# Kernel tuning notes

Measured on AMD Instinct MI355X. Metric: run time of the kernel, lower is better.

## Reference

```python
import jax, jax.numpy as jnp
import numpy as np

N = 4096       # nodes
E = 131072     # edges (avg degree 32)
IN_C = 512
HID = 512
OUT_C = 64
RANK = 64      # svd_q
N_DOM = 4
EPS = 1e-5     # BatchNorm eps


def setup_inputs() -> dict:
    key = jax.random.key(0)
    ks = jax.random.split(key, 12)
    x = jax.random.normal(ks[0], (N, IN_C), dtype=jnp.float32)
    row = jax.random.randint(ks[1], (E,), 0, N)
    off = jax.random.randint(ks[2], (E,), 1, N)
    col = (row + off) % N  # guarantee no pre-existing self loops
    edge_index = jnp.stack([row, col]).astype(jnp.int32)
    edge_weight = jax.random.uniform(ks[3], (E,), dtype=jnp.float32)
    y = jax.random.randint(ks[4], (N,), 0, N_DOM).astype(jnp.int32)
    W1 = jax.random.normal(ks[5], (IN_C, HID), dtype=jnp.float32) / np.sqrt(IN_C).astype(np.float32)
    b1 = jnp.zeros((HID,), jnp.float32)
    Wmu = jax.random.normal(ks[6], (HID, OUT_C), dtype=jnp.float32) / np.sqrt(HID).astype(np.float32)
    bmu = jnp.zeros((OUT_C,), jnp.float32)
    Wlv = jax.random.normal(ks[7], (HID, OUT_C), dtype=jnp.float32) / np.sqrt(HID).astype(np.float32)
    blv = jnp.zeros((OUT_C,), jnp.float32)
    gamma = jnp.ones((N_DOM, HID), jnp.float32)   # per-domain BN weight
    beta = jnp.zeros((N_DOM, HID), jnp.float32)   # per-domain BN bias
    return dict(x=x, edge_index=edge_index, edge_weight=edge_weight, y=y,
                W1=W1, b1=b1, Wmu=Wmu, bmu=bmu, Wlv=Wlv, blv=blv,
                gamma=gamma, beta=beta)


def _safe_rsqrt(deg):
    # PyG gcn_norm: deg^-0.5 with inf (and here non-positive) masked to 0
    safe = jnp.where(deg > 0, deg, 1.0)
    return jnp.where(deg > 0, 1.0 / jnp.sqrt(safe), 0.0)


def gcn_conv_edges(x, W, b, row, col, w, n):
    # GCNConv with edge weights: add remaining self loops (fill=1), symmetric norm
    loop = jnp.arange(n, dtype=row.dtype)
    row_f = jnp.concatenate([row, loop])
    col_f = jnp.concatenate([col, loop])
    w_f = jnp.concatenate([w, jnp.ones((n,), w.dtype)])
    deg = jax.ops.segment_sum(w_f, col_f, num_segments=n)
    dinv = _safe_rsqrt(deg)
    norm = dinv[row_f] * w_f * dinv[col_f]
    xw = x @ W                                   # [n, out]
    out = jax.ops.segment_sum(norm[:, None] * xw[row_f], col_f, num_segments=n)
    return out + b


def gcn_conv_dense(x, W, b, A):
    # Dense-adjacency GCNConv (reconstructed adjacency already has a diagonal,
    # so add_remaining_self_loops is a no-op). deg over target (col) index.
    deg = A.sum(axis=0)
    dinv = _safe_rsqrt(deg)
    Ahat = dinv[:, None] * A * dinv[None, :]     # [n, n] normalized
    return Ahat.T @ (x @ W) + b                  # aggregate at targets


def svd_lowrank_recon(A, q, niter=2):
    # torch.svd_lowrank-style randomized SVD, then U @ diag(s) @ V^T
    omega = jax.random.normal(jax.random.key(42), (A.shape[1], q), A.dtype)
    Qb = jnp.linalg.qr(A @ omega)[0]
    for _ in range(niter):
        Qb = jnp.linalg.qr(A.T @ Qb)[0]
        Qb = jnp.linalg.qr(A @ Qb)[0]
    B = Qb.T @ A                                 # [q, n]
    U, s, Vt = jnp.linalg.svd(B, full_matrices=False)
    return (Qb @ (U * s)) @ Vt                   # [n, n] low-rank reconstruction


def dsbn_relu(x, y, gamma, beta):
    # Domain-specific BatchNorm (training-mode batch stats per domain) + ReLU
    out = jnp.zeros_like(x)
    for i in range(N_DOM):
        m = (y == i)
        mf = m.astype(x.dtype)[:, None]
        cnt = jnp.maximum(mf.sum(), 1.0)
        mean = (x * mf).sum(0) / cnt
        var = (((x - mean) ** 2) * mf).sum(0) / cnt   # biased var, as BatchNorm
        xn = (x - mean) / jnp.sqrt(var + EPS) * gamma[i] + beta[i]
        out = jnp.where(m[:, None], xn, out)
    return jax.nn.relu(out)


def reference(x, edge_index, edge_weight, y, W1, b1, Wmu, bmu, Wlv, blv, gamma, beta):
    row, col = edge_index[0], edge_index[1]
    # ----- branch 1: original sparse graph -----
    h1 = dsbn_relu(gcn_conv_edges(x, W1, b1, row, col, edge_weight, N), y, gamma, beta)
    z_mean1 = gcn_conv_edges(h1, Wmu, bmu, row, col, edge_weight, N)
    z_log1 = gcn_conv_edges(h1, Wlv, blv, row, col, edge_weight, N)
    # ----- branch 2: SVD low-rank reconstructed (dense) graph -----
    A = jnp.zeros((N, N), x.dtype).at[row, col].add(edge_weight)  # coalesced COO
    A2 = svd_lowrank_recon(A, RANK)
    h2 = dsbn_relu(gcn_conv_dense(x, W1, b1, A2), y, gamma, beta)
    z_mean2 = gcn_conv_dense(h2, Wmu, bmu, A2)
    z_log2 = gcn_conv_dense(h2, Wlv, blv, A2)
    return (z_mean1, z_log1, z_mean2, z_log2)
```

## Files before the change

kernel.cpp:

```cpp
#include <hip/hip_runtime.h>
#include <hip/hip_bf16.h>


#define NN    4096
#define NEDG  131072
#define INC   512
#define HIDC  512
#define OUTC  64
#define RK    64
#define NDOM  4
#define EPSBN 1e-5f

typedef unsigned short ushortT;
typedef __attribute__((ext_vector_type(8))) short bf16x8;
typedef __attribute__((ext_vector_type(4))) float f32x4;

static inline int cdiv(int a, int b){ return (a + b - 1) / b; }

__device__ __forceinline__ float bf2f(unsigned u){ return __uint_as_float(u << 16); }

__global__ __launch_bounds__(256) void k_detect(const unsigned short* __restrict__ p,
                                                int* __restrict__ flag){
  int t = threadIdx.x;
  int cnt = 0;
  for (int i = t; i < 4096; i += 256){
    unsigned short v = p[2*i];
    int e = (v >> 7) & 0xFF;
    if (e >= 100 && e <= 140) cnt++;
  }
  __shared__ int sh[256];
  sh[t] = cnt; __syncthreads();
  for (int off = 128; off > 0; off >>= 1){ if (t < off) sh[t] += sh[t+off]; __syncthreads(); }
  if (t == 0) *flag = (sh[0] >= 2048) ? 0 : 1;
}

__device__ __forceinline__ float upc1(const void* s, int f, int off){
  return f ? ((const float*)s)[off]
           : __bfloat162float(((const __hip_bfloat16*)s)[off]);
}
__device__ __forceinline__ ushortT tobf(float v){
  __hip_bfloat16 h = __float2bfloat16(v);
  return *(ushortT*)&h;
}
#define SEG_X   2097152
#define SEG_W1  262144
#define SEG_W   131072
#define SEG_WMU 32768
#define SEG_GB  2048
#define SEG_B1  512
#define SEG_BO  64
#define OFF1 (SEG_X)
#define OFF2 (OFF1+SEG_W1)
#define OFF3 (OFF2+SEG_W)
#define OFF4 (OFF3+SEG_WMU)
#define OFF5 (OFF4+SEG_WMU)
#define OFF6 (OFF5+SEG_GB)
#define OFF7 (OFF6+SEG_GB)
#define OFF8 (OFF7+SEG_B1)
#define OFF9 (OFF8+SEG_BO)
#define OFFT (OFF9+SEG_BO)

__global__ __launch_bounds__(256) void k_upcast_all(
    const void* x, const void* W1, const void* w, const void* Wmu, const void* Wlv,
    const void* gm, const void* bt, const void* b1, const void* bmu, const void* blv,
    const int* __restrict__ isf32,
    float* dx, float* dW1, float* dw, float* dWmu, float* dWlv,
    float* dgm, float* dbt, float* db1, float* dbmu, float* dblv,
    ushortT* xbf, ushortT* W1bf, ushortT* Wmubf, ushortT* Wlvbf){
  int i = blockIdx.x*256 + threadIdx.x;
  if (i >= OFFT) return;
  int f = *isf32;
  if      (i < OFF1){ float v = upc1(x, f, i); dx[i] = v; xbf[i] = tobf(v); }
  else if (i < OFF2){ float v = upc1(W1, f, i - OFF1); dW1[i - OFF1] = v; W1bf[i - OFF1] = tobf(v); }
  else if (i < OFF3) dw  [i - OFF2] = upc1(w,   f, i - OFF2);
  else if (i < OFF4){ float v = upc1(Wmu, f, i - OFF3); dWmu[i - OFF3] = v; Wmubf[i - OFF3] = tobf(v); }
  else if (i < OFF5){ float v = upc1(Wlv, f, i - OFF4); dWlv[i - OFF4] = v; Wlvbf[i - OFF4] = tobf(v); }
  else if (i < OFF6) dgm [i - OFF5] = upc1(gm,  f, i - OFF5);
  else if (i < OFF7) dbt [i - OFF6] = upc1(bt,  f, i - OFF6);
  else if (i < OFF8) db1 [i - OFF7] = upc1(b1,  f, i - OFF7);
  else if (i < OFF9) dbmu[i - OFF8] = upc1(bmu, f, i - OFF8);
  else               dblv[i - OFF9] = upc1(blv, f, i - OFF9);
}

__global__ __launch_bounds__(256) void k_prep(float* deg, int* cntR, int* cntC, int* dcnt,
                                              float* bnsum){
  int i = blockIdx.x*256 + threadIdx.x;
  if (i < NN){ deg[i] = 1.0f; cntR[i] = 0; cntC[i] = 0; }
  if (i < NDOM) dcnt[i] = 0;
  if (i < 8*HIDC) bnsum[i] = 0.f;
}

__global__ __launch_bounds__(256) void k_hist(const int* __restrict__ row, const int* __restrict__ col,
                                              const float* __restrict__ w, float* deg,
                                              int* cntR, int* cntC){
  int e = blockIdx.x*256 + threadIdx.x;
  if (e < NEDG){
    atomicAdd(&deg[col[e]], w[e]);
    atomicAdd(&cntR[row[e]], 1);
    atomicAdd(&cntC[col[e]], 1);
  }
}
__global__ __launch_bounds__(256) void k_dinv(const float* deg, float* dinv, int n){
  int i = blockIdx.x*256 + threadIdx.x;
  if (i < n){ float d = deg[i]; dinv[i] = (d > 0.f) ? 1.f/sqrtf(d) : 0.f; }
}
__global__ __launch_bounds__(256) void k_norm1(const int* __restrict__ row, const int* __restrict__ col,
                                               const float* __restrict__ w, const float* __restrict__ dinv,
                                               float* __restrict__ nrm){
  int e = blockIdx.x*256 + threadIdx.x;
  if (e < NEDG) nrm[e] = dinv[row[e]] * w[e] * dinv[col[e]];
}
__global__ __launch_bounds__(1024) void k_scan4096(const int* __restrict__ cnt,
                                                   int* __restrict__ ptr, int* __restrict__ pos){
  __shared__ int sh[1024];
  int t = threadIdx.x;
  int b = t*4;
  int a0 = cnt[b], a1 = cnt[b+1], a2 = cnt[b+2], a3 = cnt[b+3];
  sh[t] = a0 + a1 + a2 + a3;
  __syncthreads();
  for (int off = 1; off < 1024; off <<= 1){
    int v = (t >= off) ? sh[t-off] : 0;
    __syncthreads();
    sh[t] += v;
    __syncthreads();
  }
  int excl = (t == 0) ? 0 : sh[t-1];
  ptr[b]   = excl;            pos[b]   = excl;
  ptr[b+1] = excl+a0;         pos[b+1] = excl+a0;
  ptr[b+2] = excl+a0+a1;      pos[b+2] = excl+a0+a1;
  ptr[b+3] = excl+a0+a1+a2;   pos[b+3] = excl+a0+a1+a2;
  if (t == 1023) ptr[4096] = sh[1023];
}
__global__ __launch_bounds__(256) void k_scatter(const int* __restrict__ row, const int* __restrict__ col,
                                                 int* posR, int* posC, int* eidR, int* eidC){
  int e = blockIdx.x*256 + threadIdx.x;
  if (e < NEDG){
    int p = atomicAdd(&posR[row[e]], 1); eidR[p] = e;
    int q = atomicAdd(&posC[col[e]], 1); eidC[q] = e;
  }
}
__global__ __launch_bounds__(256) void k_edges(const int* __restrict__ rowA, const int* __restrict__ colA,
        const float* __restrict__ wf, const float* __restrict__ nrm,
        const int* __restrict__ eidR, const int* __restrict__ eidC,
        int* __restrict__ csrSrc, float* __restrict__ csrW,
        int* __restrict__ cscSrc, float* __restrict__ cscW, float* __restrict__ cscN){
  int p = blockIdx.x*256 + threadIdx.x;
  if (p < NEDG){
    int eR = eidR[p]; csrSrc[p] = colA[eR]; csrW[p] = wf[eR];
    int eC = eidC[p]; cscSrc[p] = rowA[eC]; cscW[p] = wf[eC]; cscN[p] = nrm[eC];
  }
}
__global__ __launch_bounds__(256) void k_dcnt(const int* __restrict__ y, int* dcnt){
  int i = blockIdx.x*256 + threadIdx.x;
  if (i < NN) atomicAdd(&dcnt[y[i]], 1);
}

__device__ __forceinline__ unsigned rotl32(unsigned x, unsigned d){ return (x << d) | (x >> (32u - d)); }
#define TF_ROUND4(R0,R1,R2,R3) \
  x0 += x1; x1 = rotl32(x1,R0); x1 ^= x0; \
  x0 += x1; x1 = rotl32(x1,R1); x1 ^= x0; \
  x0 += x1; x1 = rotl32(x1,R2); x1 ^= x0; \
  x0 += x1; x1 = rotl32(x1,R3); x1 ^= x0;

__device__ __forceinline__ void tf2x32(unsigned k0, unsigned k1, unsigned c0, unsigned c1,
                                       unsigned* o0, unsigned* o1){
  unsigned ks2 = 0x1BD11BDAu ^ k0 ^ k1;
  unsigned x0 = c0 + k0, x1 = c1 + k1;
  TF_ROUND4(13,15,26,6);   x0 += k1;  x1 += ks2 + 1u;
  TF_ROUND4(17,29,16,24);  x0 += ks2; x1 += k0 + 2u;
  TF_ROUND4(13,15,26,6);   x0 += k0;  x1 += k1 + 3u;
  TF_ROUND4(17,29,16,24);  x0 += k1;  x1 += ks2 + 4u;
  TF_ROUND4(13,15,26,6);   x0 += ks2; x1 += k0 + 5u;
  *o0 = x0; *o1 = x1;
}

__device__ double erfinv64(double x){
  double w = -log1p(-x*x);
  double p;
  if (w < 5.0){
    w -= 2.5;
    p = 2.81022636e-08;  p = p*w + 3.43273939e-07; p = p*w - 3.5233877e-06;
    p = p*w - 4.39150654e-06; p = p*w + 0.00021858087; p = p*w - 0.00125372503;
    p = p*w - 0.00417768164;  p = p*w + 0.246640727;   p = p*w + 1.50140941;
  } else {
    w = sqrt(w) - 3.0;
    p = -0.000200214257; p = p*w + 0.000100950558; p = p*w + 0.00134934322;
    p = p*w - 0.00367342844; p = p*w + 0.00573950773; p = p*w - 0.0076224613;
    p = p*w + 0.00943887047; p = p*w + 1.00167406;    p = p*w + 2.83297682;
  }
  double y = p * x;
  const double c = 1.1283791670955126;
  #pragma unroll
  for (int it = 0; it < 3; it++){
    double err = erf(y) - x;
    y -= err / (c * exp(-y*y));
  }
  return y;
}

__device__ float bits_to_normal(unsigned b){
  float f = __uint_as_float((b >> 9) | 0x3f800000u) - 1.0f;
  const float lo = -0.99999994f;
  float x = fmaxf(lo, f * 2.0f + lo);
  double r = 1.4142135623730951 * erfinv64((double)x);
  return (float)r;
}

__global__ __launch_bounds__(256) void k_omega(float* __restrict__ om, double* __restrict__ Gd){
  int i = blockIdx.x*256 + threadIdx.x;
  if (i < RK*RK) Gd[i] = 0.0;
  if (i >= 262144) return;
  unsigned o0, o1;
  tf2x32(0u, 42u, 0u, (unsigned)i, &o0, &o1);
  om[i] = bits_to_normal(o0 ^ o1);
}

__global__ __launch_bounds__(256) void k_gemm_bf16(
    const ushortT* __restrict__ A, const ushortT* __restrict__ B,
    ushortT* __restrict__ Cbf){
  __shared__ ushortT As2[64][40];
  __shared__ ushortT Bs2[64][40];
  int t = threadIdx.x;
  int bm = blockIdx.y * 64, bn = blockIdx.x * 64;
  int w = t >> 6, l = t & 63;
  int lr = l & 15, lk = l >> 4;
  f32x4 acc[4] = {};
  int ar = t >> 2, ac = (t & 3) * 8;
  int bc = t & 63, bk = (t >> 6) * 8;
  for (int k0 = 0; k0 < 512; k0 += 32){
    *(uint4*)&As2[ar][ac] = *(const uint4*)&A[(size_t)(bm + ar) * 512 + k0 + ac];
    ushortT tmp[8];
    #pragma unroll
    for (int j = 0; j < 8; j++)
      tmp[j] = B[(size_t)(k0 + bk + j) * 512 + bn + bc];
    *(uint4*)&Bs2[bc][bk] = *(uint4*)tmp;
    __syncthreads();
    bf16x8 afrag = *(bf16x8*)&As2[w * 16 + lr][lk * 8];
    #pragma unroll
    for (int nt = 0; nt < 4; nt++){
      bf16x8 bfrag = *(bf16x8*)&Bs2[nt * 16 + lr][lk * 8];
      acc[nt] = __builtin_amdgcn_mfma_f32_16x16x32_bf16(afrag, bfrag, acc[nt], 0, 0, 0);
    }
    __syncthreads();
  }
  #pragma unroll
  for (int nt = 0; nt < 4; nt++){
    #pragma unroll
    for (int i = 0; i < 4; i++){
      size_t idx = (size_t)(bm + w * 16 + lk * 4 + i) * 512 + bn + nt * 16 + lr;
      Cbf[idx] = tobf(acc[nt][i]);
    }
  }
}

__device__ __forceinline__ void d_hw2(int bx, int t,
    const ushortT* __restrict__ A, const ushortT* __restrict__ Bm,
    const ushortT* __restrict__ Bl, float* __restrict__ Ca, float* __restrict__ Cb){
  __shared__ ushortT As2[64][40];
  __shared__ ushortT Bs2[64][40];
  int nb = NN/64;
  int second = bx >= nb;
  int bm = (bx - (second ? nb : 0)) * 64;
  const ushortT* B = second ? Bl : Bm;
  float* Cc = second ? Cb : Ca;
  int w = t >> 6, l = t & 63;
  int lr = l & 15, lk = l >> 4;
  f32x4 acc[4] = {};
  int ar = t >> 2, ac = (t & 3) * 8;
  int bc = t & 63, bk = (t >> 6) * 8;
  for (int k0 = 0; k0 < 512; k0 += 32){
    *(uint4*)&As2[ar][ac] = *(const uint4*)&A[(size_t)(bm + ar) * 512 + k0 + ac];
    ushortT tmp[8];
    #pragma unroll
    for (int j = 0; j < 8; j++)
      tmp[j] = B[(size_t)(k0 + bk + j) * 64 + bc];
    *(uint4*)&Bs2[bc][bk] = *(uint4*)tmp;
    __syncthreads();
    bf16x8 afrag = *(bf16x8*)&As2[w * 16 + lr][lk * 8];
    #pragma unroll
    for (int nt = 0; nt < 4; nt++){
      bf16x8 bfrag = *(bf16x8*)&Bs2[nt * 16 + lr][lk * 8];
      acc[nt] = __builtin_amdgcn_mfma_f32_16x16x32_bf16(afrag, bfrag, acc[nt], 0, 0, 0);
    }
    __syncthreads();
  }
  #pragma unroll
  for (int nt = 0; nt < 4; nt++){
    #pragma unroll
    for (int i = 0; i < 4; i++){
      Cc[(size_t)(bm + w * 16 + lk * 4 + i) * 64 + nt * 16 + lr] = acc[nt][i];
    }
  }
}
__global__ __launch_bounds__(256) void k_gemm_hw2(
    const ushortT* __restrict__ A, const ushortT* __restrict__ Bm,
    const ushortT* __restrict__ Bl, float* __restrict__ Ca, float* __restrict__ Cb){
  d_hw2(blockIdx.x, threadIdx.x, A, Bm, Bl, Ca, Cb);
}

__global__ __launch_bounds__(256) void k_gemm_nn(int M, int Nn, int K,
      const float* __restrict__ A, int lda, const float* __restrict__ B, int ldb,
      float* __restrict__ Cc, int ldc, const float* __restrict__ rowscale,
      const float* __restrict__ kscale, const float* __restrict__ bias){
  __shared__ float As[16][65];
  __shared__ float Bs[16][65];
  int bm = blockIdx.y*64, bn = blockIdx.x*64;
  int t = threadIdx.x;
  int tr = t >> 4, tc = t & 15;
  float acc[4][4] = {};
  for (int k0 = 0; k0 < K; k0 += 16){
    #pragma unroll
    for (int q = 0; q < 4; q++){
      int idx = t*4 + q;
      int m = idx >> 4, kk = idx & 15;
      As[kk][m] = A[(size_t)(bm+m)*lda + (k0+kk)];
    }
    #pragma unroll
    for (int q = 0; q < 4; q++){
      int idx = t + q*256;
      int kk = idx >> 6, n = idx & 63;
      float ks = kscale ? kscale[k0+kk] : 1.0f;
      Bs[kk][n] = B[(size_t)(k0+kk)*ldb + (bn+n)] * ks;
    }
    __syncthreads();
    #pragma unroll
    for (int kk = 0; kk < 16; kk++){
      float a0 = As[kk][tr*4+0], a1 = As[kk][tr*4+1], a2 = As[kk][tr*4+2], a3 = As[kk][tr*4+3];
      float b0 = Bs[kk][tc*4+0], b1 = Bs[kk][tc*4+1], b2 = Bs[kk][tc*4+2], b3 = Bs[kk][tc*4+3];
      acc[0][0] += a0*b0; acc[0][1] += a0*b1; acc[0][2] += a0*b2; acc[0][3] += a0*b3;
      acc[1][0] += a1*b0; acc[1][1] += a1*b1; acc[1][2] += a1*b2; acc[1][3] += a1*b3;
      acc[2][0] += a2*b0; acc[2][1] += a2*b1; acc[2][2] += a2*b2; acc[2][3] += a2*b3;
      acc[3][0] += a3*b0; acc[3][1] += a3*b1; acc[3][2] += a3*b2; acc[3][3] += a3*b3;
    }
    __syncthreads();
  }
  #pragma unroll
  for (int i2 = 0; i2 < 4; i2++){
    int m = bm + tr*4 + i2;
    float rs = rowscale ? rowscale[m] : 1.0f;
    #pragma unroll
    for (int j2 = 0; j2 < 4; j2++){
      int n = bn + tc*4 + j2;
      float v = acc[i2][j2] * rs;
      if (bias) v += bias[n];
      Cc[(size_t)m*ldc + n] = v;
    }
  }
}

__global__ __launch_bounds__(256) void k_gemm_nn2(
      const float* __restrict__ A, const float* __restrict__ Um,
      const float* __restrict__ rowscale,
      const float* __restrict__ bmu, const float* __restrict__ blv,
      float* __restrict__ zout){
  __shared__ float As[16][65];
  __shared__ float Bs[16][65];
  int z = blockIdx.z;
  const float* B = Um + (size_t)z*RK*RK;
  const float* bias = z ? blv : bmu;
  float* Cc = zout + (size_t)(2+z)*NN*OUTC;
  int bm = blockIdx.y*64;
  int t = threadIdx.x;
  int tr = t >> 4, tc = t & 15;
  float acc[4][4] = {};
  for (int k0 = 0; k0 < RK; k0 += 16){
    #pragma unroll
    for (int q = 0; q < 4; q++){
      int idx = t*4 + q;
      int m = idx >> 4, kk = idx & 15;
      As[kk][m] = A[(size_t)(bm+m)*RK + (k0+kk)];
    }
    #pragma unroll
    for (int q = 0; q < 4; q++){
      int idx = t + q*256;
      int kk = idx >> 6, n = idx & 63;
      Bs[kk][n] = B[(size_t)(k0+kk)*RK + n];
    }
    __syncthreads();
    #pragma unroll
    for (int kk = 0; kk < 16; kk++){
      float a0 = As[kk][tr*4+0], a1 = As[kk][tr*4+1], a2 = As[kk][tr*4+2], a3 = As[kk][tr*4+3];
      float b0 = Bs[kk][tc*4+0], b1 = Bs[kk][tc*4+1], b2 = Bs[kk][tc*4+2], b3 = Bs[kk][tc*4+3];
      acc[0][0] += a0*b0; acc[0][1] += a0*b1; acc[0][2] += a0*b2; acc[0][3] += a0*b3;
      acc[1][0] += a1*b0; acc[1][1] += a1*b1; acc[1][2] += a1*b2; acc[1][3] += a1*b3;
      acc[2][0] += a2*b0; acc[2][1] += a2*b1; acc[2][2] += a2*b2; acc[2][3] += a2*b3;
      acc[3][0] += a3*b0; acc[3][1] += a3*b1; acc[3][2] += a3*b2; acc[3][3] += a3*b3;
    }
    __syncthreads();
  }
  #pragma unroll
  for (int i2 = 0; i2 < 4; i2++){
    int m = bm + tr*4 + i2;
    float rs = rowscale[m];
    #pragma unroll
    for (int j2 = 0; j2 < 4; j2++){
      int n = tc*4 + j2;
      Cc[(size_t)m*OUTC + n] = acc[i2][j2] * rs + bias[n];
    }
  }
}

__global__ __launch_bounds__(256) void k_gemm_tn_bfm(
    const float* __restrict__ Bf1, const float* __restrict__ dinv2,
    const ushortT* __restrict__ xw1bf, float* __restrict__ Tm){
  __shared__ ushortT As2[64][40];
  __shared__ ushortT Bs2[64][40];
  int t = threadIdx.x;
  int bn = blockIdx.x * 64;
  int kb = blockIdx.y * 512;
  int w = t >> 6, l = t & 63;
  int lr = l & 15, lk = l >> 4;
  f32x4 acc[4] = {};
  int sc = t & 63, sk = (t >> 6) * 8;
  for (int k0 = kb; k0 < kb + 512; k0 += 32){
    ushortT tmpA[8], tmpB[8];
    #pragma unroll
    for (int j = 0; j < 8; j++){
      int krow = k0 + sk + j;
      tmpA[j] = tobf(dinv2[krow] * Bf1[(size_t)krow*RK + sc]);
      tmpB[j] = xw1bf[(size_t)krow*HIDC + bn + sc];
    }
    *(uint4*)&As2[sc][sk] = *(uint4*)tmpA;
    *(uint4*)&Bs2[sc][sk] = *(uint4*)tmpB;
    __syncthreads();
    bf16x8 afrag = *(bf16x8*)&As2[w*16 + lr][lk*8];
    #pragma unroll
    for (int nt = 0; nt < 4; nt++){
      bf16x8 bfrag = *(bf16x8*)&Bs2[nt*16 + lr][lk*8];
      acc[nt] = __builtin_amdgcn_mfma_f32_16x16x32_bf16(afrag, bfrag, acc[nt], 0, 0, 0);
    }
    __syncthreads();
  }
  #pragma unroll
  for (int nt = 0; nt < 4; nt++){
    #pragma unroll
    for (int i = 0; i < 4; i++){
      atomicAdd(&Tm[(size_t)(w*16 + lk*4 + i)*HIDC + bn + nt*16 + lr], acc[nt][i]);
    }
  }
}

__global__ __launch_bounds__(256) void k_gemm_tn_sk2(
      const float* __restrict__ A,
      const float* __restrict__ Ba, const float* __restrict__ Bb,
      float* __restrict__ Um, const float* __restrict__ kscale){
  __shared__ float As[32][17];
  __shared__ float Bs[32][17];
  int z = blockIdx.z;
  int second = z >= 16;
  int kb = (second ? z - 16 : z) * 256, ke = kb + 256;
  const float* B = second ? Bb : Ba;
  float* Cc = Um + (second ? RK*RK : 0);
  int bm = blockIdx.y*16, bn = blockIdx.x*16;
  int t = threadIdx.x;
  int tm = t >> 4, tn = t & 15;
  float acc = 0.f;
  for (int k0 = kb; k0 < ke; k0 += 32){
    #pragma unroll
    for (int q = 0; q < 2; q++){
      int idx = t + q*256;
      int kk = idx >> 4, m = idx & 15;
      As[kk][m] = A[(size_t)(k0+kk)*RK + (bm+m)] * kscale[k0+kk];
      Bs[kk][m] = B[(size_t)(k0+kk)*OUTC + (bn+m)];
    }
    __syncthreads();
    #pragma unroll
    for (int kk = 0; kk < 32; kk++) acc += As[kk][tm] * Bs[kk][tn];
    __syncthreads();
  }
  atomicAdd(&Cc[(size_t)(bm+tm)*RK + (bn+tn)], acc);
}

__global__ __launch_bounds__(64) void k_spmm32(const int* __restrict__ ptr,
                       const int* __restrict__ src, const float* __restrict__ cf,
                       const float* __restrict__ X, float* __restrict__ Y){
  int seg = blockIdx.x;
  int t = threadIdx.x;
  double acc = 0.0;
  int p0 = ptr[seg], p1 = ptr[seg+1];
  for (int p = p0; p < p1; ++p){
    acc += (double)cf[p] * (double)X[(size_t)src[p]*RK + t];
  }
  Y[(size_t)seg*RK + t] = (float)acc;
}
__global__ __launch_bounds__(64) void k_spmm32to64(const int* __restrict__ ptr,
                       const int* __restrict__ src, const float* __restrict__ cf,
                       const float* __restrict__ X, double* __restrict__ Y){
  int seg = blockIdx.x;
  int t = threadIdx.x;
  double acc = 0.0;
  int p0 = ptr[seg], p1 = ptr[seg+1];
  for (int p = p0; p < p1; ++p){
    acc += (double)cf[p] * (double)X[(size_t)src[p]*RK + t];
  }
  Y[(size_t)seg*RK + t] = acc;
}
__global__ __launch_bounds__(256) void k_gram64(const double* __restrict__ X, double* __restrict__ G){
  __shared__ double Xs[64][65];
  int b = blockIdx.x;
  int t = threadIdx.x;
  #pragma unroll
  for (int q = 0; q < 16; q++){
    int idx = t + q*256;
    Xs[idx >> 6][idx & 63] = X[(size_t)(b*64 + (idx >> 6))*RK + (idx & 63)];
  }
  __syncthreads();
  int i = t >> 2;
  int j0 = (t & 3) * 16;
  double acc[16];
  #pragma unroll
  for (int jj = 0; jj < 16; jj++) acc[jj] = 0.0;
  for (int k = 0; k < 64; k++){
    double a = Xs[k][i];
    #pragma unroll
    for (int jj = 0; jj < 16; jj++) acc[jj] += a * Xs[k][j0+jj];
  }
  #pragma unroll
  for (int jj = 0; jj < 16; jj++) atomicAdd(&G[i*RK + j0 + jj], acc[jj]);
}

#define CHOLF_CHUNK(I0) \
  for (int k2 = 0; k2 < 16; k2++){ \
    int k = (I0) + k2; \
    int buf = k & 1; \
    if (t < 64 && j == k){ \
      double d = sqrt(fmax(cdiag, 1e-300)); \
      double s = 1.0 / d; \
      myd = d; \
      sdd[k] = s; \
      _Pragma("unroll") \
      for (int i = (I0); i < 64; i++){ c[i] *= s; colk[buf][i] = c[i]; } \
    } \
    __syncthreads(); \
    if (t < 64 && j > k && j < 64){ \
      double cj = colk[buf][j]; \
      cdiag -= cj * cj; \
      _Pragma("unroll") \
      for (int i = (I0); i < 64; i++){ c[i] -= colk[buf][i] * cj; } \
    } \
    __syncthreads(); \
  }

__global__ __launch_bounds__(256) void k_chol_spmm(
    double* __restrict__ G, double* __restrict__ sdd,
    const int* __restrict__ ptr, const int* __restrict__ src, const float* __restrict__ cf,
    const ushortT* __restrict__ Xb, float* __restrict__ Y,
    const float* __restrict__ self_dinv, const float* __restrict__ bias){
  __shared__ double colk[2][64];
  int t = threadIdx.x;
  if (blockIdx.x == 0){
    int j = t;
    double c[64];
    double cdiag = 0.0, myd = 0.0;
    if (t < 64){
      #pragma unroll
      for (int i = 0; i < 64; i++) c[i] = G[i*64 + j];
      #pragma unroll
      for (int i = 0; i < 64; i++) if (i == j) cdiag = c[i];
    }
    CHOLF_CHUNK(0)
    CHOLF_CHUNK(16)
    CHOLF_CHUNK(32)
    CHOLF_CHUNK(48)
    if (t < 64){
      #pragma unroll
      for (int i = 0; i < 64; i++){
        double v = (i > j) ? c[i] : 0.0;
        if (i == j) v = myd;
        G[i*64 + j] = v;
      }
    }
  } else {
    int seg = blockIdx.x - 1;
    float acc0, acc1;
    {
      float sd = self_dinv[seg]; float s2 = sd*sd;
      unsigned v = *(const unsigned*)&Xb[(size_t)seg*HIDC + 2*t];
      acc0 = s2 * bf2f(v & 0xffffu);
      acc1 = s2 * bf2f(v >> 16);
    }
    int p0 = ptr[seg], p1 = ptr[seg+1];
    for (int p = p0; p < p1; ++p){
      int o = src[p];
      float cc = cf[p];
      unsigned v = *(const unsigned*)&Xb[(size_t)o*HIDC + 2*t];
      acc0 += cc * bf2f(v & 0xffffu);
      acc1 += cc * bf2f(v >> 16);
    }
    acc0 += bias[2*t];
    acc1 += bias[2*t+1];
    Y[(size_t)seg*HIDC + 2*t]     = acc0;
    Y[(size_t)seg*HIDC + 2*t + 1] = acc1;
  }
}

__device__ __forceinline__ void d_bnpart(int b, int t,
    const float* __restrict__ H, const int* __restrict__ y, float* __restrict__ bnsum){
  int j0 = 2*t;
  float s00=0,s01=0,s10=0,s11=0,s20=0,s21=0,s30=0,s31=0;
  float q00=0,q01=0,q10=0,q11=0,q20=0,q21=0,q30=0,q31=0;
  int r0 = b*32;
  for (int r = r0; r < r0+32; r++){
    int d = y[r];
    float2 v = *(const float2*)&H[(size_t)r*HIDC + j0];
    float ax = v.x, ay = v.y;
    float bx = ax*ax, by = ay*ay;
    if      (d == 0){ s00+=ax; s01+=ay; q00+=bx; q01+=by; }
    else if (d == 1){ s10+=ax; s11+=ay; q10+=bx; q11+=by; }
    else if (d == 2){ s20+=ax; s21+=ay; q20+=bx; q21+=by; }
    else            { s30+=ax; s31+=ay; q30+=bx; q31+=by; }
  }
  atomicAdd(&bnsum[0*HIDC+j0], s00); atomicAdd(&bnsum[0*HIDC+j0+1], s01);
  atomicAdd(&bnsum[1*HIDC+j0], s10); atomicAdd(&bnsum[1*HIDC+j0+1], s11);
  atomicAdd(&bnsum[2*HIDC+j0], s20); atomicAdd(&bnsum[2*HIDC+j0+1], s21);
  atomicAdd(&bnsum[3*HIDC+j0], s30); atomicAdd(&bnsum[3*HIDC+j0+1], s31);
  atomicAdd(&bnsum[4*HIDC+j0], q00); atomicAdd(&bnsum[4*HIDC+j0+1], q01);
  atomicAdd(&bnsum[5*HIDC+j0], q10); atomicAdd(&bnsum[5*HIDC+j0+1], q11);
  atomicAdd(&bnsum[6*HIDC+j0], q20); atomicAdd(&bnsum[6*HIDC+j0+1], q21);
  atomicAdd(&bnsum[7*HIDC+j0], q30); atomicAdd(&bnsum[7*HIDC+j0+1], q31);
}
__global__ __launch_bounds__(256) void k_bnpart(const float* __restrict__ H,
        const int* __restrict__ y, float* __restrict__ bnsum){
  d_bnpart(blockIdx.x, threadIdx.x, H, y, bnsum);
}

__device__ __forceinline__ void d_bnapply(int idx,
    const float* __restrict__ H, const int* __restrict__ y,
    const float* __restrict__ bnsum, const int* __restrict__ dcnt,
    const float* __restrict__ gamma, const float* __restrict__ beta,
    ushortT* __restrict__ Hbf){
  int n = idx >> 9, j = idx & (HIDC-1);
  int d = y[n];
  float cnt  = fmaxf((float)dcnt[d], 1.0f);
  float mean = bnsum[d*HIDC + j] / cnt;
  float var  = fmaxf(bnsum[(4+d)*HIDC + j] / cnt - mean*mean, 0.f);
  float inv  = 1.0f / sqrtf(var + EPSBN);
  float gmm  = gamma[d*HIDC + j];
  float scal = gmm * inv;
  float shft = beta[d*HIDC + j] - mean * gmm * inv;
  float v = H[idx] * scal + shft;
  v = v > 0.f ? v : 0.f;
  Hbf[idx] = tobf(v);
}
__global__ __launch_bounds__(256) void k_bnapply(const float* __restrict__ H, const int* __restrict__ y,
        const float* __restrict__ bnsum, const int* __restrict__ dcnt,
        const float* __restrict__ gamma, const float* __restrict__ beta,
        ushortT* __restrict__ Hbf){
  int idx = blockIdx.x*256 + threadIdx.x;
  if (idx < NN*HIDC) d_bnapply(idx, H, y, bnsum, dcnt, gamma, beta, Hbf);
}

__global__ __launch_bounds__(256) void k_trinv_bn(const double* __restrict__ L,
      const double* __restrict__ sdd, double* __restrict__ Rinv,
      const float* __restrict__ H, const int* __restrict__ y, float* __restrict__ bnsum){
  int t = threadIdx.x;
  if (blockIdx.x > 0){
    d_bnpart(blockIdx.x - 1, t, H, y, bnsum);
    return;
  }
  __shared__ double gl[64][65];
  __shared__ double Xl[64][65];
  __shared__ double sdinv[64];
  __shared__ double Sl[3][16][17];
  #pragma unroll
  for (int q = 0; q < 16; q++){
    int idx = t + (q << 8);
    gl[idx >> 6][idx & 63] = L[idx];
  }
  if (t < 64) sdinv[t] = sdd[t];
  for (int idx = t; idx < 64*65; idx += 256)
    ((double*)Xl)[idx] = 0.0;
  __syncthreads();
  if (t < 64){
    int b = t >> 4, c2 = t & 15;
    int g0 = b << 4;
    int gc = g0 + c2;
    Xl[gc][gc] = sdinv[gc];
    for (int i = c2 - 1; i >= 0; i--){
      int gi = g0 + i;
      double s = 0.0;
      for (int k2 = i + 1; k2 <= c2; k2++)
        s += gl[g0 + k2][gi] * Xl[g0 + k2][gc];
      Xl[gi][gc] = -s * sdinv[gi];
    }
  }
  __syncthreads();
  for (int d = 1; d < 4; d++){
    int np = 4 - d;
    int tot = np << 8;
    for (int e = t; e < tot; e += 256){
      int p = e >> 8;
      int i = (e >> 4) & 15, jj = e & 15;
      int gi = (p << 4) + i, gj = ((p + d) << 4) + jj;
      double s = 0.0;
      int a0 = (p + 1) << 4, a1 = (p + d + 1) << 4;
      for (int a = a0; a < a1; a++)
        s += gl[a][gi] * Xl[a][gj];
      Sl[p][i][jj] = s;
    }
    __syncthreads();
    for (int e = t; e < tot; e += 256){
      int p = e >> 8;
      int i = (e >> 4) & 15, jj = e & 15;
      int gi = (p << 4) + i, gj = ((p + d) << 4) + jj;
      double s = 0.0;
      #pragma unroll
      for (int k2 = 0; k2 < 16; k2++)
        s += Xl[gi][(p << 4) + k2] * Sl[p][k2][jj];
      Xl[gi][gj] = -s;
    }
    __syncthreads();
  }
  #pragma unroll
  for (int q = 0; q < 16; q++){
    int e2 = t + (q << 8);
    Rinv[e2] = Xl[e2 >> 6][e2 & 63];
  }
}

__global__ __launch_bounds__(256) void k_applyR_bn(const double* __restrict__ srcQ,
      const double* __restrict__ Rinv, double* __restrict__ dst, float* __restrict__ Bf1,
      const float* __restrict__ H, const int* __restrict__ y,
      const float* __restrict__ bnsum, const int* __restrict__ dcnt,
      const float* __restrict__ gamma, const float* __restrict__ beta,
      ushortT* __restrict__ Hbf){
  int t = threadIdx.x;
  if (blockIdx.x >= NN/4){
    int idx = (blockIdx.x - NN/4)*256 + t;
    if (idx < NN*HIDC) d_bnapply(idx, H, y, bnsum, dcnt, gamma, beta, Hbf);
    return;
  }
  __shared__ double Rs[64][65];
  #pragma unroll
  for (int q = 0; q < 16; q++){
    int idx = t + q*256;
    Rs[idx >> 6][idx & 63] = Rinv[idx];
  }
  __syncthreads();
  int r = blockIdx.x*4 + (t >> 6);
  int j = t & 63;
  const double* rowp = srcQ + (size_t)r*RK;
  double s = 0.0;
  for (int k = 0; k <= j; k++) s += rowp[k] * Rs[k][j];
  dst[(size_t)r*RK + j] = s;
  Bf1[(size_t)r*RK + j] = (float)s;
}

__global__ __launch_bounds__(256) void k_qsum_spmmC_hw2(
    const double* __restrict__ Q, double* __restrict__ qs,
    const int* __restrict__ ptr, const int* __restrict__ src, const float* __restrict__ cf,
    const float* __restrict__ Xf, float* __restrict__ Cm,
    const ushortT* __restrict__ A, const ushortT* __restrict__ Bm,
    const ushortT* __restrict__ Bl, float* __restrict__ Ca, float* __restrict__ Cb){
  int t = threadIdx.x;
  if (blockIdx.x < 64){
    int j = blockIdx.x;
    double a = 0.0;
    for (int n = t; n < NN; n += 256) a += Q[(size_t)n*RK + j];
    __shared__ double sh[256];
    sh[t] = a; __syncthreads();
    for (int off = 128; off > 0; off >>= 1){ if (t < off) sh[t] += sh[t+off]; __syncthreads(); }
    if (t == 0) qs[j] = sh[0];
    return;
  }
  if (blockIdx.x < 64 + NN/4){
    int seg = (blockIdx.x - 64)*4 + (t >> 6);
    int lane = t & 63;
    double acc = 0.0;
    int p0 = ptr[seg], p1 = ptr[seg+1];
    for (int p = p0; p < p1; ++p){
      acc += (double)cf[p] * (double)Xf[(size_t)src[p]*RK + lane];
    }
    Cm[(size_t)seg*RK + lane] = (float)acc;
    return;
  }
  d_hw2(blockIdx.x - 64 - NN/4, t, A, Bm, Bl, Ca, Cb);
}

__global__ void k_fin_spmm2(
    const float* __restrict__ Cm, const double* __restrict__ qs, float* __restrict__ dinv2,
    float* __restrict__ Tm, float* __restrict__ Um, float* __restrict__ bnsum,
    const int* __restrict__ ptr, const int* __restrict__ src, const float* __restrict__ cf,
    const float* __restrict__ Xa, const float* __restrict__ Xb2,
    float* __restrict__ zout, const float* __restrict__ self_dinv,
    const float* __restrict__ bmu, const float* __restrict__ blv){
  int t = threadIdx.x;
  if (blockIdx.x < 128){
    int idx = blockIdx.x*256 + t;
    Tm[idx] = 0.f;
    if (idx < 2*RK*RK) Um[idx] = 0.f;
    if (idx < 8*HIDC)  bnsum[idx] = 0.f;
    if (idx < NN){
      double s = 0.0;
      #pragma unroll
      for (int k = 0; k < RK; k++) s += (double)Cm[(size_t)idx*RK + k] * qs[k];
      dinv2[idx] = (s > 0.0) ? (float)(1.0/sqrt(s)) : 0.f;
    }
    return;
  }
  int bb = blockIdx.x - 128;
  int second = bb >= NN/4;
  int seg = (second ? bb - NN/4 : bb)*4 + (t >> 6);
  int lane = t & 63;
  const float* X = second ? Xb2 : Xa;
  const float* bias = second ? blv : bmu;
  float* Y = zout + (second ? (size_t)NN*OUTC : 0);
  float acc0;
  {
    float sd = self_dinv[seg];
    acc0 = sd*sd * X[(size_t)seg*OUTC + lane];
  }
  int p0 = ptr[seg], p1 = ptr[seg+1];
  for (int p = p0; p < p1; ++p){
    acc0 += cf[p] * X[(size_t)src[p]*OUTC + lane];
  }
  acc0 += bias[lane];
  Y[(size_t)seg*OUTC + lane] = acc0;
}

extern "C" void kernel_launch(void* const* d_in, const int* in_sizes, int n_in,
                              void* d_out, int out_size, void* d_ws, size_t ws_size,
                              hipStream_t stream){
  (void)in_sizes; (void)n_in; (void)out_size;
  const void* x_in  = d_in[0];
  const int*  ei    = (const int*)d_in[1];
  const void* w_in  = d_in[2];
  const int*  yv    = (const int*)d_in[3];
  const void* W1i   = d_in[4];
  const void* b1i   = d_in[5];
  const void* Wmui  = d_in[6];
  const void* bmui  = d_in[7];
  const void* Wlvi  = d_in[8];
  const void* blvi  = d_in[9];
  const void* gmi   = d_in[10];
  const void* bti   = d_in[11];
  const int* rowA = ei;
  const int* colA = ei + NEDG;
  float* zout = (float*)d_out;

  double* Dp = (double*)d_ws;
  size_t od = 0;
  double* Qd0 = Dp + od; od += (size_t)NN*RK;
  double* Qd1 = Dp + od; od += (size_t)NN*RK;
  double* Gd  = Dp + od; od += RK*RK;
  double* Rid = Dp + od; od += RK*RK;
  double* qsd = Dp + od; od += RK;
  double* sdd = Dp + od; od += RK;
  float* Fp = (float*)(Dp + od);
  size_t o = 0;
  float* xf   = Fp + o; o += (size_t)NN*INC;
  float* W1f  = Fp + o; o += (size_t)INC*HIDC;
  float* b1f  = Fp + o; o += HIDC;
  float* Wmuf = Fp + o; o += (size_t)HIDC*OUTC;
  float* bmuf = Fp + o; o += OUTC;
  float* Wlvf = Fp + o; o += (size_t)HIDC*OUTC;
  float* blvf = Fp + o; o += OUTC;
  float* gmf  = Fp + o; o += NDOM*HIDC;
  float* btf  = Fp + o; o += NDOM*HIDC;
  float* wf   = Fp + o; o += NEDG;
  float* hwA  = Fp + o; o += (size_t)NN*OUTC;
  float* hwB  = Fp + o; o += (size_t)NN*OUTC;
  float* Bf1  = Fp + o; o += (size_t)NN*RK;
  float* Cm   = Fp + o; o += (size_t)NN*RK;
  float* Qf0  = Fp + o; o += (size_t)NN*RK;
  float* Qf1  = Fp + o; o += (size_t)NN*RK;
  float* Tm   = Fp + o; o += (size_t)RK*HIDC;
  float* Umu  = Fp + o; o += 2*RK*RK;
  float* deg1 = Fp + o; o += NN;
  float* dinv1= Fp + o; o += NN;
  float* dinv2= Fp + o; o += NN;
  float* norm1= Fp + o; o += NEDG;
  float* bnsum= Fp + o; o += 8*HIDC;
  float* csrW = Fp + o; o += NEDG;
  float* cscW = Fp + o; o += NEDG;
  float* cscN = Fp + o; o += NEDG;
  ushortT* xbf   = (ushortT*)(Fp + o); o += (size_t)NN*INC/2;
  ushortT* W1bf  = (ushortT*)(Fp + o); o += (size_t)INC*HIDC/2;
  ushortT* xw1bf = (ushortT*)(Fp + o); o += (size_t)NN*HIDC/2;
  ushortT* hbf   = (ushortT*)(Fp + o); o += (size_t)NN*HIDC/2;
  ushortT* Wmubf = (ushortT*)(Fp + o); o += (size_t)HIDC*OUTC/2;
  ushortT* Wlvbf = (ushortT*)(Fp + o); o += (size_t)HIDC*OUTC/2;
  int* Ip = (int*)(Fp + o);
  size_t oi = 0;
  int* cntR = Ip + oi; oi += NN;
  int* ptrR = Ip + oi; oi += NN + 1;
  int* posR = Ip + oi; oi += NN;
  int* eidR = Ip + oi; oi += NEDG;
  int* cntC = Ip + oi; oi += NN;
  int* ptrC = Ip + oi; oi += NN + 1;
  int* posC = Ip + oi; oi += NN;
  int* eidC = Ip + oi; oi += NEDG;
  int* csrSrc = Ip + oi; oi += NEDG;
  int* cscSrc = Ip + oi; oi += NEDG;
  int* dcnt = Ip + oi; oi += NDOM;
  int* dflag= Ip + oi; oi += 1;

  size_t need = od*sizeof(double) + o*sizeof(float) + (oi+16)*sizeof(int);
  if (ws_size < need) return;

  float* hbuf = xf;

  const int T = 256;
  k_detect<<<1,T,0,stream>>>((const unsigned short*)x_in, dflag);
  k_upcast_all<<<cdiv(OFFT,T),T,0,stream>>>(
      x_in, W1i, w_in, Wmui, Wlvi, gmi, bti, b1i, bmui, blvi, dflag,
      xf, W1f, wf, Wmuf, Wlvf, gmf, btf, b1f, bmuf, blvf,
      xbf, W1bf, Wmubf, Wlvbf);

  k_prep<<<cdiv(NN,T),T,0,stream>>>(deg1, cntR, cntC, dcnt, bnsum);
  k_hist <<<cdiv(NEDG,T),T,0,stream>>>(rowA, colA, wf, deg1, cntR, cntC);
  k_dinv <<<cdiv(NN,T),T,0,stream>>>(deg1, dinv1, NN);
  k_norm1<<<cdiv(NEDG,T),T,0,stream>>>(rowA, colA, wf, dinv1, norm1);
  k_scan4096<<<1,1024,0,stream>>>(cntR, ptrR, posR);
  k_scan4096<<<1,1024,0,stream>>>(cntC, ptrC, posC);
  k_scatter<<<cdiv(NEDG,T),T,0,stream>>>(rowA, colA, posR, posC, eidR, eidC);
  k_edges<<<cdiv(NEDG,T),T,0,stream>>>(rowA, colA, wf, norm1, eidR, eidC,
                                       csrSrc, csrW, cscSrc, cscW, cscN);
  k_omega<<<cdiv(NN*RK,T),T,0,stream>>>(Qf0, Gd);
  k_dcnt <<<cdiv(NN,T),T,0,stream>>>(yv, dcnt);

  k_gemm_bf16<<<dim3(HIDC/64, NN/64),256,0,stream>>>(xbf, W1bf, xw1bf);

  k_spmm32<<<NN,64,0,stream>>>(ptrR, csrSrc, csrW, Qf0, Qf1);
  k_spmm32<<<NN,64,0,stream>>>(ptrC, cscSrc, cscW, Qf1, Qf0);
  k_spmm32<<<NN,64,0,stream>>>(ptrR, csrSrc, csrW, Qf0, Qf1);
  k_spmm32<<<NN,64,0,stream>>>(ptrC, cscSrc, cscW, Qf1, Qf0);
  k_spmm32to64<<<NN,64,0,stream>>>(ptrR, csrSrc, csrW, Qf0, Qd1);
  k_gram64<<<NN/64,256,0,stream>>>(Qd1, Gd);

  k_chol_spmm<<<NN+1,256,0,stream>>>(Gd, sdd, ptrC, cscSrc, cscN, xw1bf, hbuf,
                                     dinv1, b1f);
  k_trinv_bn<<<1+NN/32,256,0,stream>>>(Gd, sdd, Rid, hbuf, yv, bnsum);
  k_applyR_bn<<<NN/4 + cdiv(NN*HIDC,T),256,0,stream>>>(Qd1, Rid, Qd0, Bf1,
      hbuf, yv, bnsum, dcnt, gmf, btf, hbf);
  k_qsum_spmmC_hw2<<<64 + NN/4 + 2*(NN/64),256,0,stream>>>(Qd0, qsd,
      ptrC, cscSrc, cscW, Bf1, Cm, hbf, Wmubf, Wlvbf, hwA, hwB);
  k_fin_spmm2<<<128 + 2*(NN/4),256,0,stream>>>(Cm, qsd, dinv2, Tm, Umu, bnsum,
      ptrC, cscSrc, cscN, hwA, hwB, zout, dinv1, bmuf, blvf);

  k_gemm_tn_bfm<<<dim3(HIDC/64, 8),256,0,stream>>>(Bf1, dinv2, xw1bf, Tm);
  k_gemm_nn<<<dim3(HIDC/64, NN/64),256,0,stream>>>(NN,HIDC,RK, Cm,RK, Tm,HIDC, hbuf,HIDC, dinv2, nullptr, b1f);
  k_bnpart<<<NN/32,256,0,stream>>>(hbuf, yv, bnsum);
  k_bnapply<<<cdiv(NN*HIDC,T),T,0,stream>>>(hbuf, yv, bnsum, dcnt, gmf, btf, hbf);
  k_gemm_hw2<<<2*(NN/64),256,0,stream>>>(hbf, Wmubf, Wlvbf, hwA, hwB);
  k_gemm_tn_sk2<<<dim3(RK/16, RK/16, 32),256,0,stream>>>(Bf1, hwA, hwB, Umu, dinv2);
  k_gemm_nn2<<<dim3(1, NN/64, 2),256,0,stream>>>(Cm, Umu, dinv2, bmuf, blvf, zout);
}
```

Baseline: 530.2 us.

## Reassociate dense-branch output GEMMs and merge small launches

```diff
diff --git a/kernel.cpp b/kernel.cpp
--- a/kernel.cpp
+++ b/kernel.cpp
@@ -110,9 +110,13 @@
   int e = blockIdx.x*256 + threadIdx.x;
   if (e < NEDG) nrm[e] = dinv[row[e]] * w[e] * dinv[col[e]];
 }
-__global__ __launch_bounds__(1024) void k_scan4096(const int* __restrict__ cnt,
-                                                   int* __restrict__ ptr, int* __restrict__ pos){
+__global__ __launch_bounds__(1024) void k_scan2(
+    const int* __restrict__ cntR, int* __restrict__ ptrR, int* __restrict__ posR,
+    const int* __restrict__ cntC, int* __restrict__ ptrC, int* __restrict__ posC){
   __shared__ int sh[1024];
+  const int* cnt = blockIdx.x ? cntC : cntR;
+  int* ptr = blockIdx.x ? ptrC : ptrR;
+  int* pos = blockIdx.x ? posC : posR;
   int t = threadIdx.x;
   int b = t*4;
   int a0 = cnt[b], a1 = cnt[b+1], a2 = cnt[b+2], a3 = cnt[b+3];
@@ -206,22 +210,11 @@
   return (float)r;
 }
 
-__global__ __launch_bounds__(256) void k_omega(float* __restrict__ om, double* __restrict__ Gd){
-  int i = blockIdx.x*256 + threadIdx.x;
-  if (i < RK*RK) Gd[i] = 0.0;
-  if (i >= 262144) return;
-  unsigned o0, o1;
-  tf2x32(0u, 42u, 0u, (unsigned)i, &o0, &o1);
-  om[i] = bits_to_normal(o0 ^ o1);
-}
-
-__global__ __launch_bounds__(256) void k_gemm_bf16(
+__device__ __forceinline__ void d_gemm_bf16(int bm, int bn, int t,
     const ushortT* __restrict__ A, const ushortT* __restrict__ B,
     ushortT* __restrict__ Cbf){
   __shared__ ushortT As2[64][40];
   __shared__ ushortT Bs2[64][40];
-  int t = threadIdx.x;
-  int bm = blockIdx.y * 64, bn = blockIdx.x * 64;
   int w = t >> 6, l = t & 63;
   int lr = l & 15, lk = l >> 4;
   f32x4 acc[4] = {};
@@ -251,6 +244,22 @@
       Cbf[idx] = tobf(acc[nt][i]);
     }
   }
+}
+
+__global__ __launch_bounds__(256) void k_omega_gemm(
+    float* __restrict__ om, double* __restrict__ Gd,
+    const ushortT* __restrict__ A, const ushortT* __restrict__ B,
+    ushortT* __restrict__ Cbf){
+  if (blockIdx.x < 1024){
+    int i = blockIdx.x*256 + threadIdx.x;
+    if (i < RK*RK) Gd[i] = 0.0;
+    unsigned o0, o1;
+    tf2x32(0u, 42u, 0u, (unsigned)i, &o0, &o1);
+    om[i] = bits_to_normal(o0 ^ o1);
+    return;
+  }
+  int bx = blockIdx.x - 1024;
+  d_gemm_bf16((bx >> 3) * 64, (bx & 7) * 64, threadIdx.x, A, B, Cbf);
 }
 
 __device__ __forceinline__ void d_hw2(int bx, int t,
@@ -292,11 +301,6 @@
     }
   }
 }
-__global__ __launch_bounds__(256) void k_gemm_hw2(
-    const ushortT* __restrict__ A, const ushortT* __restrict__ Bm,
-    const ushortT* __restrict__ Bl, float* __restrict__ Ca, float* __restrict__ Cb){
-  d_hw2(blockIdx.x, threadIdx.x, A, Bm, Bl, Ca, Cb);
-}
 
 __global__ __launch_bounds__(256) void k_gemm_nn(int M, int Nn, int K,
       const float* __restrict__ A, int lda, const float* __restrict__ B, int ldb,
@@ -402,7 +406,7 @@
 
 __global__ __launch_bounds__(256) void k_gemm_tn_bfm(
     const float* __restrict__ Bf1, const float* __restrict__ dinv2,
-    const ushortT* __restrict__ xw1bf, float* __restrict__ Tm){
+    const ushortT* __restrict__ Bbf, float* __restrict__ Out){
   __shared__ ushortT As2[64][40];
   __shared__ ushortT Bs2[64][40];
   int t = threadIdx.x;
@@ -418,7 +422,7 @@
     for (int j = 0; j < 8; j++){
       int krow = k0 + sk + j;
       tmpA[j] = tobf(dinv2[krow] * Bf1[(size_t)krow*RK + sc]);
-      tmpB[j] = xw1bf[(size_t)krow*HIDC + bn + sc];
+      tmpB[j] = Bbf[(size_t)krow*HIDC + bn + sc];
     }
     *(uint4*)&As2[sc][sk] = *(uint4*)tmpA;
     *(uint4*)&Bs2[sc][sk] = *(uint4*)tmpB;
@@ -435,40 +439,55 @@
   for (int nt = 0; nt < 4; nt++){
     #pragma unroll
     for (int i = 0; i < 4; i++){
-      atomicAdd(&Tm[(size_t)(w*16 + lk*4 + i)*HIDC + bn + nt*16 + lr], acc[nt][i]);
-    }
-  }
-}
-
-__global__ __launch_bounds__(256) void k_gemm_tn_sk2(
-      const float* __restrict__ A,
-      const float* __restrict__ Ba, const float* __restrict__ Bb,
-      float* __restrict__ Um, const float* __restrict__ kscale){
-  __shared__ float As[32][17];
-  __shared__ float Bs[32][17];
-  int z = blockIdx.z;
-  int second = z >= 16;
-  int kb = (second ? z - 16 : z) * 256, ke = kb + 256;
-  const float* B = second ? Bb : Ba;
-  float* Cc = Um + (second ? RK*RK : 0);
-  int bm = blockIdx.y*16, bn = blockIdx.x*16;
-  int t = threadIdx.x;
-  int tm = t >> 4, tn = t & 15;
-  float acc = 0.f;
-  for (int k0 = kb; k0 < ke; k0 += 32){
-    #pragma unroll
-    for (int q = 0; q < 2; q++){
+      atomicAdd(&Out[(size_t)(w*16 + lk*4 + i)*HIDC + bn + nt*16 + lr], acc[nt][i]);
+    }
+  }
+}
+
+__global__ __launch_bounds__(256) void k_gemm_tw(
+    const float* __restrict__ T2, const float* __restrict__ Wmu,
+    const float* __restrict__ Wlv, float* __restrict__ Um){
+  __shared__ float As[16][65];
+  __shared__ float Bs[16][65];
+  const float* B = blockIdx.x ? Wlv : Wmu;
+  float* Cc = Um + (blockIdx.x ? RK*RK : 0);
+  int t = threadIdx.x;
+  int tr = t >> 4, tc = t & 15;
+  float acc[4][4] = {};
+  for (int k0 = 0; k0 < HIDC; k0 += 16){
+    #pragma unroll
+    for (int q = 0; q < 4; q++){
+      int idx = t*4 + q;
+      int m = idx >> 4, kk = idx & 15;
+      As[kk][m] = T2[(size_t)m*HIDC + (k0+kk)];
+    }
+    #pragma unroll
+    for (int q = 0; q < 4; q++){
       int idx = t + q*256;
-      int kk = idx >> 4, m = idx & 15;
-      As[kk][m] = A[(size_t)(k0+kk)*RK + (bm+m)] * kscale[k0+kk];
-      Bs[kk][m] = B[(size_t)(k0+kk)*OUTC + (bn+m)];
-    }
-    __syncthreads();
-    #pragma unroll
-    for (int kk = 0; kk < 32; kk++) acc += As[kk][tm] * Bs[kk][tn];
-    __syncthreads();
-  }
-  atomicAdd(&Cc[(size_t)(bm+tm)*RK + (bn+tn)], acc);
+      int kk = idx >> 6, n = idx & 63;
+      Bs[kk][n] = B[(size_t)(k0+kk)*OUTC + n];
+    }
+    __syncthreads();
+    #pragma unroll
+    for (int kk = 0; kk < 16; kk++){
+      float a0 = As[kk][tr*4+0], a1 = As[kk][tr*4+1], a2 = As[kk][tr*4+2], a3 = As[kk][tr*4+3];
+      float b0 = Bs[kk][tc*4+0], b1 = Bs[kk][tc*4+1], b2 = Bs[kk][tc*4+2], b3 = Bs[kk][tc*4+3];
+      acc[0][0] += a0*b0; acc[0][1] += a0*b1; acc[0][2] += a0*b2; acc[0][3] += a0*b3;
+      acc[1][0] += a1*b0; acc[1][1] += a1*b1; acc[1][2] += a1*b2; acc[1][3] += a1*b3;
+      acc[2][0] += a2*b0; acc[2][1] += a2*b1; acc[2][2] += a2*b2; acc[2][3] += a2*b3;
+      acc[3][0] += a3*b0; acc[3][1] += a3*b1; acc[3][2] += a3*b2; acc[3][3] += a3*b3;
+    }
+    __syncthreads();
+  }
+  #pragma unroll
+  for (int i2 = 0; i2 < 4; i2++){
+    int m = tr*4 + i2;
+    #pragma unroll
+    for (int j2 = 0; j2 < 4; j2++){
+      int n = tc*4 + j2;
+      Cc[(size_t)m*RK + n] = acc[i2][j2];
+    }
+  }
 }
 
 __global__ __launch_bounds__(64) void k_spmm32(const int* __restrict__ ptr,
@@ -779,7 +798,8 @@
 
 __global__ void k_fin_spmm2(
     const float* __restrict__ Cm, const double* __restrict__ qs, float* __restrict__ dinv2,
-    float* __restrict__ Tm, float* __restrict__ Um, float* __restrict__ bnsum,
+    float* __restrict__ Tm, float* __restrict__ T2, float* __restrict__ Um,
+    float* __restrict__ bnsum,
     const int* __restrict__ ptr, const int* __restrict__ src, const float* __restrict__ cf,
     const float* __restrict__ Xa, const float* __restrict__ Xb2,
     float* __restrict__ zout, const float* __restrict__ self_dinv,
@@ -788,6 +808,7 @@
   if (blockIdx.x < 128){
     int idx = blockIdx.x*256 + t;
     Tm[idx] = 0.f;
+    T2[idx] = 0.f;
     if (idx < 2*RK*RK) Um[idx] = 0.f;
     if (idx < 8*HIDC)  bnsum[idx] = 0.f;
     if (idx < NN){
@@ -865,6 +886,7 @@
   float* Qf0  = Fp + o; o += (size_t)NN*RK;
   float* Qf1  = Fp + o; o += (size_t)NN*RK;
   float* Tm   = Fp + o; o += (size_t)RK*HIDC;
+  float* T2   = Fp + o; o += (size_t)RK*HIDC;
   float* Umu  = Fp + o; o += 2*RK*RK;
   float* deg1 = Fp + o; o += NN;
   float* dinv1= Fp + o; o += NN;
@@ -911,15 +933,13 @@
   k_hist <<<cdiv(NEDG,T),T,0,stream>>>(rowA, colA, wf, deg1, cntR, cntC);
   k_dinv <<<cdiv(NN,T),T,0,stream>>>(deg1, dinv1, NN);
   k_norm1<<<cdiv(NEDG,T),T,0,stream>>>(rowA, colA, wf, dinv1, norm1);
-  k_scan4096<<<1,1024,0,stream>>>(cntR, ptrR, posR);
-  k_scan4096<<<1,1024,0,stream>>>(cntC, ptrC, posC);
+  k_scan2<<<2,1024,0,stream>>>(cntR, ptrR, posR, cntC, ptrC, posC);
   k_scatter<<<cdiv(NEDG,T),T,0,stream>>>(rowA, colA, posR, posC, eidR, eidC);
   k_edges<<<cdiv(NEDG,T),T,0,stream>>>(rowA, colA, wf, norm1, eidR, eidC,
                                        csrSrc, csrW, cscSrc, cscW, cscN);
-  k_omega<<<cdiv(NN*RK,T),T,0,stream>>>(Qf0, Gd);
   k_dcnt <<<cdiv(NN,T),T,0,stream>>>(yv, dcnt);
 
-  k_gemm_bf16<<<dim3(HIDC/64, NN/64),256,0,stream>>>(xbf, W1bf, xw1bf);
+  k_omega_gemm<<<1024 + 512,256,0,stream>>>(Qf0, Gd, xbf, W1bf, xw1bf);
 
   k_spmm32<<<NN,64,0,stream>>>(ptrR, csrSrc, csrW, Qf0, Qf1);
   k_spmm32<<<NN,64,0,stream>>>(ptrC, cscSrc, cscW, Qf1, Qf0);
@@ -935,14 +955,14 @@
       hbuf, yv, bnsum, dcnt, gmf, btf, hbf);
   k_qsum_spmmC_hw2<<<64 + NN/4 + 2*(NN/64),256,0,stream>>>(Qd0, qsd,
       ptrC, cscSrc, cscW, Bf1, Cm, hbf, Wmubf, Wlvbf, hwA, hwB);
-  k_fin_spmm2<<<128 + 2*(NN/4),256,0,stream>>>(Cm, qsd, dinv2, Tm, Umu, bnsum,
+  k_fin_spmm2<<<128 + 2*(NN/4),256,0,stream>>>(Cm, qsd, dinv2, Tm, T2, Umu, bnsum,
       ptrC, cscSrc, cscN, hwA, hwB, zout, dinv1, bmuf, blvf);
 
   k_gemm_tn_bfm<<<dim3(HIDC/64, 8),256,0,stream>>>(Bf1, dinv2, xw1bf, Tm);
   k_gemm_nn<<<dim3(HIDC/64, NN/64),256,0,stream>>>(NN,HIDC,RK, Cm,RK, Tm,HIDC, hbuf,HIDC, dinv2, nullptr, b1f);
   k_bnpart<<<NN/32,256,0,stream>>>(hbuf, yv, bnsum);
   k_bnapply<<<cdiv(NN*HIDC,T),T,0,stream>>>(hbuf, yv, bnsum, dcnt, gmf, btf, hbf);
-  k_gemm_hw2<<<2*(NN/64),256,0,stream>>>(hbf, Wmubf, Wlvbf, hwA, hwB);
-  k_gemm_tn_sk2<<<dim3(RK/16, RK/16, 32),256,0,stream>>>(Bf1, hwA, hwB, Umu, dinv2);
+  k_gemm_tn_bfm<<<dim3(HIDC/64, 8),256,0,stream>>>(Bf1, dinv2, hbf, T2);
+  k_gemm_tw<<<2,256,0,stream>>>(T2, Wmuf, Wlvf, Umu);
   k_gemm_nn2<<<dim3(1, NN/64, 2),256,0,stream>>>(Cm, Umu, dinv2, bmuf, blvf, zout);
 }
```

Result: no change. 533.1 us (+0.5%).
